# Kernel tuning notes

Hardware: AMD Instinct MI355X
Metric: run time of the kernel (lower is better)

## Reference

```python
import jax, jax.numpy as jnp
import numpy as np

N_EMBD = 1568  # 2 * 784, hard-coded in the source module
HEAD_SIZE = 128
BATCH = 16384


def setup_inputs() -> dict:
    key = jax.random.key(0)
    kx, kq, kk, kv = jax.random.split(key, 4)
    x = jax.random.normal(kx, (BATCH, N_EMBD), dtype=jnp.float32)
    wq = jax.random.normal(kq, (N_EMBD, HEAD_SIZE), dtype=jnp.float32) * (N_EMBD ** -0.5)
    wk = jax.random.normal(kk, (N_EMBD, HEAD_SIZE), dtype=jnp.float32) * (N_EMBD ** -0.5)
    wv = jax.random.normal(kv, (N_EMBD, HEAD_SIZE), dtype=jnp.float32) * (N_EMBD ** -0.5)
    return {"x": x, "wq": wq, "wk": wk, "wv": wv}


def reference(x, wq, wk, wv):
    # x: [B, N]; projections (bias-free Linear): [B, H]
    B, N = x.shape
    q = x @ wq
    k = x @ wk
    v = x @ wv
    # Outer-product score matrix per batch element: [B, H, H]
    attn = jnp.einsum('bi,bj->bij', q, k) * (N ** -0.5)  # scale uses FEATURE dim N, as in source
    attn = jax.nn.softmax(attn, axis=-1)
    # dropout is identity in eval mode
    out = jnp.einsum('bij,bj->bi', attn, v)  # [B, H]
    return out
```

## Files before the change

### kernel.cpp

```cpp
#include <hip/hip_runtime.h>
#include <stdint.h>

typedef unsigned short u16;
typedef __bf16 bf16x8 __attribute__((ext_vector_type(8)));
typedef float f32x4 __attribute__((ext_vector_type(4)));

#define M_ROWS 16384
#define K_DIM  1568
#define H_DIM  128
#define MT     32
#define BK     32
#define NITER  49
#define ASTR   36
#define PSTR   132
#define SCALE  0.02525381361380526f
#define LOG2E  1.4426950408889634f

__device__ __forceinline__ u16 f32_to_bf16_rne(float f) {
    uint32_t u = __float_as_uint(f);
    uint32_t r = (u + 0x7FFFu + ((u >> 16) & 1u)) >> 16;
    return (u16)r;
}

__global__ __launch_bounds__(256) void wtrans_kernel(
    const float* __restrict__ wq, const float* __restrict__ wk,
    const float* __restrict__ wv, u16* __restrict__ wt)
{
    __shared__ u16 tile[32][33];
    const float* w = (blockIdx.z == 0) ? wq : (blockIdx.z == 1) ? wk : wv;
    const int k0 = blockIdx.x * 32;
    const int n0 = blockIdx.y * 32;

    const int tn = threadIdx.x & 31;
    const int tk = threadIdx.x >> 5;
    #pragma unroll
    for (int p = 0; p < 4; p++) {
        int kk = tk + p * 8;
        tile[kk][tn] = f32_to_bf16_rne(w[(size_t)(k0 + kk) * H_DIM + n0 + tn]);
    }
    __syncthreads();

    u16* dst = wt + (size_t)blockIdx.z * H_DIM * K_DIM;
    const int tk2 = threadIdx.x & 31;
    const int tn2 = threadIdx.x >> 5;
    #pragma unroll
    for (int p = 0; p < 4; p++) {
        int nn = tn2 + p * 8;
        dst[(size_t)(n0 + nn) * K_DIM + k0 + tk2] = tile[tk2][nn];
    }
}

__global__ __launch_bounds__(512) void fused_kernel(
    const float* __restrict__ x,
    const u16* __restrict__ wt,
    float* __restrict__ out)
{
    __shared__ u16   As[2][MT * ASTR];
    __shared__ float Pq[MT][PSTR];
    __shared__ float Pk[MT][PSTR];
    __shared__ float Pv[MT][PSTR];

    const int tid  = threadIdx.x;
    const int lane = tid & 63;
    const int wave = tid >> 6;
    const int lrow = lane & 15;
    const int quad = lane >> 4;
    const int m0   = blockIdx.x * MT;

    const int srow = tid >> 4;
    const int scol = tid & 15;
    const float* aptr = x + (size_t)(m0 + srow) * K_DIM + scol * 2;

    const u16* bp[3];
    #pragma unroll
    for (int nt = 0; nt < 3; nt++) {
        int ng = wave * 48 + nt * 16 + lrow;
        bp[nt] = wt + (size_t)(ng >> 7) * (H_DIM * K_DIM)
                    + (size_t)(ng & 127) * K_DIM + quad * 8;
    }

    {
        float2 a0 = *(const float2*)(aptr);
        uint32_t p = (uint32_t)f32_to_bf16_rne(a0.x)
                   | ((uint32_t)f32_to_bf16_rne(a0.y) << 16);
        ((uint32_t*)&As[0][srow * ASTR])[scol] = p;
    }
    bf16x8 bcur[3];
    #pragma unroll
    for (int nt = 0; nt < 3; nt++) bcur[nt] = *(const bf16x8*)(bp[nt]);
    __syncthreads();

    f32x4 acc[2][3] = {};

    for (int kk = 0; kk < NITER; kk++) {
        const int kn = (kk < NITER - 1) ? (kk + 1) * BK : kk * BK;
        float2 an = *(const float2*)(aptr + kn);
        bf16x8 bn0 = *(const bf16x8*)(bp[0] + kn);
        bf16x8 bn1 = *(const bf16x8*)(bp[1] + kn);
        bf16x8 bn2 = *(const bf16x8*)(bp[2] + kn);

        const int buf = kk & 1;
        union { uint2 h[2]; bf16x8 v; } a0f, a1f;
        {
            const u16* ap0 = &As[buf][(0 * 16 + lrow) * ASTR + quad * 8];
            const u16* ap1 = &As[buf][(1 * 16 + lrow) * ASTR + quad * 8];
            a0f.h[0] = *(const uint2*)(ap0);
            a0f.h[1] = *(const uint2*)(ap0 + 4);
            a1f.h[0] = *(const uint2*)(ap1);
            a1f.h[1] = *(const uint2*)(ap1 + 4);
        }

        acc[0][0] = __builtin_amdgcn_mfma_f32_16x16x32_bf16(a0f.v, bcur[0], acc[0][0], 0, 0, 0);
        acc[1][0] = __builtin_amdgcn_mfma_f32_16x16x32_bf16(a1f.v, bcur[0], acc[1][0], 0, 0, 0);
        acc[0][1] = __builtin_amdgcn_mfma_f32_16x16x32_bf16(a0f.v, bcur[1], acc[0][1], 0, 0, 0);
        acc[1][1] = __builtin_amdgcn_mfma_f32_16x16x32_bf16(a1f.v, bcur[1], acc[1][1], 0, 0, 0);
        acc[0][2] = __builtin_amdgcn_mfma_f32_16x16x32_bf16(a0f.v, bcur[2], acc[0][2], 0, 0, 0);
        acc[1][2] = __builtin_amdgcn_mfma_f32_16x16x32_bf16(a1f.v, bcur[2], acc[1][2], 0, 0, 0);

        {
            uint32_t p = (uint32_t)f32_to_bf16_rne(an.x)
                       | ((uint32_t)f32_to_bf16_rne(an.y) << 16);
            ((uint32_t*)&As[buf ^ 1][srow * ASTR])[scol] = p;
        }
        __syncthreads();
        bcur[0] = bn0; bcur[1] = bn1; bcur[2] = bn2;
    }

    #pragma unroll
    for (int mt = 0; mt < 2; mt++) {
        #pragma unroll
        for (int nt = 0; nt < 3; nt++) {
            const int base = wave * 48 + nt * 16;
            const int sel  = base >> 7;
            const int col  = (base & 127) + lrow;
            const int mrow = mt * 16 + quad * 4;
            if (sel == 0) {
                #pragma unroll
                for (int r = 0; r < 4; r++)
                    Pq[mrow + r][col] = acc[mt][nt][r] * (SCALE * LOG2E);
            } else if (sel == 1) {
                #pragma unroll
                for (int r = 0; r < 4; r++)
                    Pk[mrow + r][col] = acc[mt][nt][r];
            } else {
                #pragma unroll
                for (int r = 0; r < 4; r++)
                    Pv[mrow + r][col] = acc[mt][nt][r];
            }
        }
    }
    __syncthreads();

    const int r   = tid >> 4;
    const int sub = tid & 15;

    float qq[8], num[8], den[8];
    #pragma unroll
    for (int ii = 0; ii < 8; ii++) {
        qq[ii]  = Pq[r][sub * 8 + ii];
        num[ii] = 0.f;
        den[ii] = 0.f;
    }

    #pragma unroll 4
    for (int j = 0; j < 128; j++) {
        float kj = Pk[r][j];
        float vj = Pv[r][j];
        #pragma unroll
        for (int ii = 0; ii < 8; ii++) {
            float e = __builtin_amdgcn_exp2f(qq[ii] * kj);
            den[ii] += e;
            num[ii] += e * vj;
        }
    }

    float* op = out + (size_t)(m0 + r) * H_DIM + sub * 8;
    #pragma unroll
    for (int g = 0; g < 2; g++) {
        float4 o;
        o.x = num[4 * g + 0] / den[4 * g + 0];
        o.y = num[4 * g + 1] / den[4 * g + 1];
        o.z = num[4 * g + 2] / den[4 * g + 2];
        o.w = num[4 * g + 3] / den[4 * g + 3];
        *(float4*)(op + 4 * g) = o;
    }
}

extern "C" void kernel_launch(void* const* d_in, const int* in_sizes, int n_in,
                              void* d_out, int out_size, void* d_ws, size_t ws_size,
                              hipStream_t stream)
{
    const float* x  = (const float*)d_in[0];
    const float* wq = (const float*)d_in[1];
    const float* wk = (const float*)d_in[2];
    const float* wv = (const float*)d_in[3];
    float* out = (float*)d_out;

    u16* wt = (u16*)d_ws;

    wtrans_kernel<<<dim3(K_DIM / 32, H_DIM / 32, 3), 256, 0, stream>>>(wq, wk, wv, wt);
    fused_kernel<<<M_ROWS / MT, 512, 0, stream>>>(x, wt, out);
}
```

Baseline: 240.3 us.

## Pre-convert x to bf16 in separate pass and load MFMA operands directly

Adds a kernel that converts x from fp32 to bf16 into workspace. The fused GEMM then loads A fragments straight from global memory into registers, which removes the LDS staging buffer and the per-iteration __syncthreads. In exchange x is read in fp32, written back in bf16 and read again, adding roughly 150 MB of extra traffic and one more launch. Each wave also reloads A rows redundantly from global memory or cache.

New measurement: 250.4 us. +4.2%, slower.

```diff
diff --git a/kernel.cpp b/kernel.cpp
--- a/kernel.cpp
+++ b/kernel.cpp
@@ -11,7 +11,6 @@
 #define MT     32
 #define BK     32
 #define NITER  49
-#define ASTR   36
 #define PSTR   132
 #define SCALE  0.02525381361380526f
 #define LOG2E  1.4426950408889634f
@@ -22,6 +21,22 @@
     return (u16)r;
 }
 
+#define MFMA(a, b, c) __builtin_amdgcn_mfma_f32_16x16x32_bf16(a, b, c, 0, 0, 0)
+
+__global__ __launch_bounds__(256) void xconv_kernel(
+    const float* __restrict__ x, u16* __restrict__ xb)
+{
+    size_t i = ((size_t)blockIdx.x * 256 + threadIdx.x) * 8;
+    float4 f0 = *(const float4*)(x + i);
+    float4 f1 = *(const float4*)(x + i + 4);
+    union { u16 h[8]; uint4 v; } p;
+    p.h[0] = f32_to_bf16_rne(f0.x); p.h[1] = f32_to_bf16_rne(f0.y);
+    p.h[2] = f32_to_bf16_rne(f0.z); p.h[3] = f32_to_bf16_rne(f0.w);
+    p.h[4] = f32_to_bf16_rne(f1.x); p.h[5] = f32_to_bf16_rne(f1.y);
+    p.h[6] = f32_to_bf16_rne(f1.z); p.h[7] = f32_to_bf16_rne(f1.w);
+    *(uint4*)(xb + i) = p.v;
+}
+
 __global__ __launch_bounds__(256) void wtrans_kernel(
     const float* __restrict__ wq, const float* __restrict__ wk,
     const float* __restrict__ wv, u16* __restrict__ wt)
@@ -51,11 +66,10 @@
 }
 
 __global__ __launch_bounds__(512) void fused_kernel(
-    const float* __restrict__ x,
+    const u16* __restrict__ xb,
     const u16* __restrict__ wt,
     float* __restrict__ out)
 {
-    __shared__ u16   As[2][MT * ASTR];
     __shared__ float Pq[MT][PSTR];
     __shared__ float Pk[MT][PSTR];
     __shared__ float Pv[MT][PSTR];
@@ -67,10 +81,8 @@
     const int quad = lane >> 4;
     const int m0   = blockIdx.x * MT;
 
-    const int srow = tid >> 4;
-    const int scol = tid & 15;
-    const float* aptr = x + (size_t)(m0 + srow) * K_DIM + scol * 2;
-
+    const u16* ap0 = xb + (size_t)(m0 + lrow) * K_DIM + quad * 8;
+    const u16* ap1 = ap0 + (size_t)16 * K_DIM;
     const u16* bp[3];
     #pragma unroll
     for (int nt = 0; nt < 3; nt++) {
@@ -79,52 +91,38 @@
                     + (size_t)(ng & 127) * K_DIM + quad * 8;
     }
 
-    {
-        float2 a0 = *(const float2*)(aptr);
-        uint32_t p = (uint32_t)f32_to_bf16_rne(a0.x)
-                   | ((uint32_t)f32_to_bf16_rne(a0.y) << 16);
-        ((uint32_t*)&As[0][srow * ASTR])[scol] = p;
-    }
-    bf16x8 bcur[3];
-    #pragma unroll
-    for (int nt = 0; nt < 3; nt++) bcur[nt] = *(const bf16x8*)(bp[nt]);
-    __syncthreads();
-
     f32x4 acc[2][3] = {};
 
-    for (int kk = 0; kk < NITER; kk++) {
-        const int kn = (kk < NITER - 1) ? (kk + 1) * BK : kk * BK;
-        float2 an = *(const float2*)(aptr + kn);
-        bf16x8 bn0 = *(const bf16x8*)(bp[0] + kn);
-        bf16x8 bn1 = *(const bf16x8*)(bp[1] + kn);
-        bf16x8 bn2 = *(const bf16x8*)(bp[2] + kn);
-
-        const int buf = kk & 1;
-        union { uint2 h[2]; bf16x8 v; } a0f, a1f;
-        {
-            const u16* ap0 = &As[buf][(0 * 16 + lrow) * ASTR + quad * 8];
-            const u16* ap1 = &As[buf][(1 * 16 + lrow) * ASTR + quad * 8];
-            a0f.h[0] = *(const uint2*)(ap0);
-            a0f.h[1] = *(const uint2*)(ap0 + 4);
-            a1f.h[0] = *(const uint2*)(ap1);
-            a1f.h[1] = *(const uint2*)(ap1 + 4);
-        }
-
-        acc[0][0] = __builtin_amdgcn_mfma_f32_16x16x32_bf16(a0f.v, bcur[0], acc[0][0], 0, 0, 0);
-        acc[1][0] = __builtin_amdgcn_mfma_f32_16x16x32_bf16(a1f.v, bcur[0], acc[1][0], 0, 0, 0);
-        acc[0][1] = __builtin_amdgcn_mfma_f32_16x16x32_bf16(a0f.v, bcur[1], acc[0][1], 0, 0, 0);
-        acc[1][1] = __builtin_amdgcn_mfma_f32_16x16x32_bf16(a1f.v, bcur[1], acc[1][1], 0, 0, 0);
-        acc[0][2] = __builtin_amdgcn_mfma_f32_16x16x32_bf16(a0f.v, bcur[2], acc[0][2], 0, 0, 0);
-        acc[1][2] = __builtin_amdgcn_mfma_f32_16x16x32_bf16(a1f.v, bcur[2], acc[1][2], 0, 0, 0);
-
-        {
-            uint32_t p = (uint32_t)f32_to_bf16_rne(an.x)
-                       | ((uint32_t)f32_to_bf16_rne(an.y) << 16);
-            ((uint32_t*)&As[buf ^ 1][srow * ASTR])[scol] = p;
-        }
-        __syncthreads();
-        bcur[0] = bn0; bcur[1] = bn1; bcur[2] = bn2;
-    }
+    bf16x8 a0 = *(const bf16x8*)(ap0);
+    bf16x8 a1 = *(const bf16x8*)(ap1);
+    bf16x8 b0 = *(const bf16x8*)(bp[0]);
+    bf16x8 b1 = *(const bf16x8*)(bp[1]);
+    bf16x8 b2 = *(const bf16x8*)(bp[2]);
+
+    #pragma unroll 2
+    for (int kk = 1; kk < NITER; kk++) {
+        const int ko = kk * BK;
+        bf16x8 an0 = *(const bf16x8*)(ap0 + ko);
+        bf16x8 an1 = *(const bf16x8*)(ap1 + ko);
+        bf16x8 bn0 = *(const bf16x8*)(bp[0] + ko);
+        bf16x8 bn1 = *(const bf16x8*)(bp[1] + ko);
+        bf16x8 bn2 = *(const bf16x8*)(bp[2] + ko);
+
+        acc[0][0] = MFMA(a0, b0, acc[0][0]);
+        acc[1][0] = MFMA(a1, b0, acc[1][0]);
+        acc[0][1] = MFMA(a0, b1, acc[0][1]);
+        acc[1][1] = MFMA(a1, b1, acc[1][1]);
+        acc[0][2] = MFMA(a0, b2, acc[0][2]);
+        acc[1][2] = MFMA(a1, b2, acc[1][2]);
+
+        a0 = an0; a1 = an1; b0 = bn0; b1 = bn1; b2 = bn2;
+    }
+    acc[0][0] = MFMA(a0, b0, acc[0][0]);
+    acc[1][0] = MFMA(a1, b0, acc[1][0]);
+    acc[0][1] = MFMA(a0, b1, acc[0][1]);
+    acc[1][1] = MFMA(a1, b1, acc[1][1]);
+    acc[0][2] = MFMA(a0, b2, acc[0][2]);
+    acc[1][2] = MFMA(a1, b2, acc[1][2]);
 
     #pragma unroll
     for (int mt = 0; mt < 2; mt++) {
@@ -197,7 +195,9 @@
     float* out = (float*)d_out;
 
     u16* wt = (u16*)d_ws;
+    u16* xb = (u16*)((char*)d_ws + (size_t)3 * H_DIM * K_DIM * 2);
 
     wtrans_kernel<<<dim3(K_DIM / 32, H_DIM / 32, 3), 256, 0, stream>>>(wq, wk, wv, wt);
-    fused_kernel<<<M_ROWS / MT, 512, 0, stream>>>(x, wt, out);
-}
+    xconv_kernel<<<(M_ROWS * K_DIM) / (8 * 256), 256, 0, stream>>>(x, xb);
+    fused_kernel<<<M_ROWS / MT, 512, 0, stream>>>(xb, wt, out);
+}
```
